# Kernel tuning notes

Measured on AMD Instinct MI355X. Metric: run time of the kernel, lower is better.

The kernel has to match this reference:

```python
import jax, jax.numpy as jnp
import numpy as np

TEMPERATURE = 8.0  # sqrt(d_k=64)
NEG_INF = -1.0e9   # matches masked_fill value in source


def setup_inputs() -> dict:
    key = jax.random.key(0)
    kq, kk, kv, km = jax.random.split(key, 4)
    B, H, T, C = 2, 16, 2048, 64
    q = jax.random.normal(kq, (B, H, T, C), dtype=jnp.float32)
    k = jax.random.normal(kk, (B, H, T, C), dtype=jnp.float32)
    v = jax.random.normal(kv, (B, H, T, C), dtype=jnp.float32)
    mask = jax.random.randint(km, (B, 1, T, T), 0, 2, dtype=jnp.int32)
    return {"q": q, "k": k, "v": v, "mask": mask}


def reference(q, k, v, mask):
    # attn = (q / temperature) @ k^T   -> [b, h, T, T]
    attn = jnp.einsum("bhqc,bhkc->bhqk", q / TEMPERATURE, k)
    attn = jnp.where(mask == 0, NEG_INF, attn)
    attn = jax.nn.softmax(attn, axis=-1)
    # dropout is identity in eval / deterministic reference
    output = jnp.einsum("bhqk,bhkc->bhqc", attn, v)
    return (output, attn)
```

## Files before the change

### kernel.cpp

```cpp
#include <hip/hip_runtime.h>
#include <stdint.h>
#include <stddef.h>

#define T_DIM 2048
#define C_DIM 64
#define SCALE_L2E 0.18033688011112042f

typedef __bf16 bf16x8 __attribute__((ext_vector_type(8)));
typedef float f32x4 __attribute__((ext_vector_type(4)));
typedef unsigned int u32x4 __attribute__((ext_vector_type(4)));
typedef unsigned int u32x2 __attribute__((ext_vector_type(2)));
typedef int i32x4 __attribute__((ext_vector_type(4)));
typedef unsigned short u16t;

#define PIDX(row, e) ((row) * T_DIM + ((e) ^ (((row) & 7) << 3)))

static __device__ __forceinline__ unsigned f2bf_bits(float f) {
  unsigned u = __builtin_bit_cast(unsigned, f);
  u += 0x7fffu + ((u >> 16) & 1u);
  return u >> 16;
}
static __device__ __forceinline__ bf16x8 asfrag(u32x4 u) {
  return __builtin_bit_cast(bf16x8, u);
}
static __device__ __forceinline__ bf16x8 pack8(f32x4 a, f32x4 b) {
  u32x4 u;
  u[0] = f2bf_bits(a[0]) | (f2bf_bits(a[1]) << 16);
  u[1] = f2bf_bits(a[2]) | (f2bf_bits(a[3]) << 16);
  u[2] = f2bf_bits(b[0]) | (f2bf_bits(b[1]) << 16);
  u[3] = f2bf_bits(b[2]) | (f2bf_bits(b[3]) << 16);
  return __builtin_bit_cast(bf16x8, u);
}
static __device__ __forceinline__ bf16x8 ld_cvt8(const float* p) {
  return pack8(*(const f32x4*)p, *(const f32x4*)(p + 4));
}

__global__ __launch_bounds__(256) void prep_kernel(const float* __restrict__ k,
                                                   const float* __restrict__ v,
                                                   u16t* __restrict__ kb,
                                                   u16t* __restrict__ vt) {
  if (blockIdx.x < 2048) {
    const size_t e0 = ((size_t)blockIdx.x * 256 + threadIdx.x) * 8;
    const float* src = k + e0;
    u32x4 u;
    f32x4 a = *(const f32x4*)src;
    f32x4 b = *(const f32x4*)(src + 4);
    u[0] = f2bf_bits(a[0]) | (f2bf_bits(a[1]) << 16);
    u[1] = f2bf_bits(a[2]) | (f2bf_bits(a[3]) << 16);
    u[2] = f2bf_bits(b[0]) | (f2bf_bits(b[1]) << 16);
    u[3] = f2bf_bits(b[2]) | (f2bf_bits(b[3]) << 16);
    *(u32x4*)(kb + e0) = u;
  } else {
    const int gid = (blockIdx.x - 2048) * 256 + threadIdx.x;
    const int bh = gid >> 11;
    const int j = gid & (T_DIM - 1);
    const float* src = v + ((size_t)bh * T_DIM + j) * C_DIM;
    u16t* dst = vt + (size_t)bh * (C_DIM * T_DIM) + j;
#pragma unroll
    for (int c0 = 0; c0 < C_DIM; c0 += 4) {
      f32x4 x = *(const f32x4*)(src + c0);
#pragma unroll
      for (int e = 0; e < 4; ++e)
        dst[(size_t)(c0 + e) * T_DIM] = (u16t)f2bf_bits(x[e]);
    }
  }
}

template <bool USE_PREP>
__global__ __launch_bounds__(256, 2) void attn_fwd(
    const float* __restrict__ qp, const float* __restrict__ kp,
    const float* __restrict__ vp, const int* __restrict__ maskp,
    const u16t* __restrict__ kbp, const u16t* __restrict__ vtp,
    float* __restrict__ outp, float* __restrict__ attnp) {
  __shared__ u16t Plds[16 * T_DIM];

  const int tid = threadIdx.x;
  const int wave = tid >> 6;
  const int lane = tid & 63;
  const int quad = lane >> 4;
  const int l15 = lane & 15;

  const int h = blockIdx.x & 15;
  const int qb = (blockIdx.x >> 4) & 127;
  const int b = blockIdx.x >> 11;
  const int bh = b * 16 + h;
  const int q0 = qb << 4;

  const float* qrow = qp + ((size_t)bh * T_DIM + q0 + l15) * C_DIM + quad * 8;
  const bf16x8 qf0 = ld_cvt8(qrow);
  const bf16x8 qf1 = ld_cvt8(qrow + 32);

  const u16t* kbbase = kbp + (size_t)bh * T_DIM * C_DIM;
  const float* kfbase = kp + (size_t)bh * T_DIM * C_DIM;
  const float* vfbase = vp + (size_t)bh * T_DIM * C_DIM;
  const u16t* vtrow = vtp + ((size_t)bh * C_DIM + l15) * T_DIM;
  const int* mrow = maskp + ((size_t)b * T_DIM + q0 + l15) * T_DIM;

  f32x4 ao0 = {0.f, 0.f, 0.f, 0.f};
  f32x4 ao1 = {0.f, 0.f, 0.f, 0.f};
  f32x4 ao2 = {0.f, 0.f, 0.f, 0.f};
  f32x4 ao3 = {0.f, 0.f, 0.f, 0.f};

#pragma unroll 1
  for (int s = 0; s < 16; ++s) {
    const int j0 = (s * 4 + wave) * 32;

    bf16x8 kA0, kA1, kB0, kB1;
    if (USE_PREP) {
      const u16t* ka = kbbase + (size_t)(j0 + l15) * C_DIM + quad * 8;
      kA0 = asfrag(*(const u32x4*)(ka));
      kA1 = asfrag(*(const u32x4*)(ka + 32));
      kB0 = asfrag(*(const u32x4*)(ka + 16 * C_DIM));
      kB1 = asfrag(*(const u32x4*)(ka + 16 * C_DIM + 32));
    } else {
      const float* ka = kfbase + (size_t)(j0 + l15) * C_DIM + quad * 8;
      kA0 = ld_cvt8(ka);
      kA1 = ld_cvt8(ka + 32);
      kB0 = ld_cvt8(ka + 16 * C_DIM);
      kB1 = ld_cvt8(ka + 16 * C_DIM + 32);
    }
    const i32x4 mA = *(const i32x4*)(mrow + j0 + quad * 4);
    const i32x4 mB = *(const i32x4*)(mrow + j0 + 16 + quad * 4);

    u32x4 vb0, vb1, vb2, vb3;
    if (USE_PREP) {
      const u16t* vt0 = vtrow + j0 + quad * 8;
      vb0 = *(const u32x4*)(vt0);
      vb1 = *(const u32x4*)(vt0 + 16 * T_DIM);
      vb2 = *(const u32x4*)(vt0 + 32 * T_DIM);
      vb3 = *(const u32x4*)(vt0 + 48 * T_DIM);
    } else {
      const float* g = vfbase + (size_t)(j0 + quad * 8) * C_DIM + l15;
      auto gather = [&](int c0) -> u32x4 {
        const float* p = g + c0;
        u32x4 r;
        r[0] = f2bf_bits(p[0]) | (f2bf_bits(p[C_DIM]) << 16);
        r[1] = f2bf_bits(p[2 * C_DIM]) | (f2bf_bits(p[3 * C_DIM]) << 16);
        r[2] = f2bf_bits(p[4 * C_DIM]) | (f2bf_bits(p[5 * C_DIM]) << 16);
        r[3] = f2bf_bits(p[6 * C_DIM]) | (f2bf_bits(p[7 * C_DIM]) << 16);
        return r;
      };
      vb0 = gather(0); vb1 = gather(16); vb2 = gather(32); vb3 = gather(48);
    }

    f32x4 sA = {0.f, 0.f, 0.f, 0.f};
    sA = __builtin_amdgcn_mfma_f32_16x16x32_bf16(kA0, qf0, sA, 0, 0, 0);
    sA = __builtin_amdgcn_mfma_f32_16x16x32_bf16(kA1, qf1, sA, 0, 0, 0);
    f32x4 sB = {0.f, 0.f, 0.f, 0.f};
    sB = __builtin_amdgcn_mfma_f32_16x16x32_bf16(kB0, qf0, sB, 0, 0, 0);
    sB = __builtin_amdgcn_mfma_f32_16x16x32_bf16(kB1, qf1, sB, 0, 0, 0);

    float a0 = mA[0] ? __builtin_exp2f(sA[0] * SCALE_L2E) : 0.f;
    float a1 = mA[1] ? __builtin_exp2f(sA[1] * SCALE_L2E) : 0.f;
    float a2 = mA[2] ? __builtin_exp2f(sA[2] * SCALE_L2E) : 0.f;
    float a3 = mA[3] ? __builtin_exp2f(sA[3] * SCALE_L2E) : 0.f;
    float b0 = mB[0] ? __builtin_exp2f(sB[0] * SCALE_L2E) : 0.f;
    float b1 = mB[1] ? __builtin_exp2f(sB[1] * SCALE_L2E) : 0.f;
    float b2 = mB[2] ? __builtin_exp2f(sB[2] * SCALE_L2E) : 0.f;
    float b3 = mB[3] ? __builtin_exp2f(sB[3] * SCALE_L2E) : 0.f;

    u32x2 wA, wB;
    wA[0] = f2bf_bits(a0) | (f2bf_bits(a1) << 16);
    wA[1] = f2bf_bits(a2) | (f2bf_bits(a3) << 16);
    wB[0] = f2bf_bits(b0) | (f2bf_bits(b1) << 16);
    wB[1] = f2bf_bits(b2) | (f2bf_bits(b3) << 16);
    *(u32x2*)&Plds[PIDX(l15, j0 + quad * 4)] = wA;
    *(u32x2*)&Plds[PIDX(l15, j0 + 16 + quad * 4)] = wB;

    const bf16x8 pa = asfrag(*(const u32x4*)&Plds[PIDX(l15, j0 + quad * 8)]);
    ao0 = __builtin_amdgcn_mfma_f32_16x16x32_bf16(pa, asfrag(vb0), ao0, 0, 0, 0);
    ao1 = __builtin_amdgcn_mfma_f32_16x16x32_bf16(pa, asfrag(vb1), ao1, 0, 0, 0);
    ao2 = __builtin_amdgcn_mfma_f32_16x16x32_bf16(pa, asfrag(vb2), ao2, 0, 0, 0);
    ao3 = __builtin_amdgcn_mfma_f32_16x16x32_bf16(pa, asfrag(vb3), ao3, 0, 0, 0);
  }

  __syncthreads();

  const int tq = tid >> 4;
  const int tj = (tid & 15) * 8;
  float ls = 0.f;
#pragma unroll
  for (int it = 0; it < 16; ++it) {
    const u32x4 pv = *(const u32x4*)&Plds[PIDX(tq, tj + it * 128)];
#pragma unroll
    for (int e = 0; e < 4; ++e) {
      ls += __builtin_bit_cast(float, pv[e] << 16);
      ls += __builtin_bit_cast(float, pv[e] & 0xffff0000u);
    }
  }
  ls += __shfl_xor(ls, 1, 64);
  ls += __shfl_xor(ls, 2, 64);
  ls += __shfl_xor(ls, 4, 64);
  ls += __shfl_xor(ls, 8, 64);
  const float rl = 1.0f / ls;

  float* arow = attnp + ((size_t)bh * T_DIM + q0 + tq) * T_DIM;
#pragma unroll
  for (int it = 0; it < 16; ++it) {
    const int j = tj + it * 128;
    const u32x4 pv = *(const u32x4*)&Plds[PIDX(tq, j)];
    f32x4 o0, o1;
#pragma unroll
    for (int e = 0; e < 2; ++e) {
      o0[2 * e] = __builtin_bit_cast(float, pv[e] << 16) * rl;
      o0[2 * e + 1] = __builtin_bit_cast(float, pv[e] & 0xffff0000u) * rl;
      o1[2 * e] = __builtin_bit_cast(float, pv[e + 2] << 16) * rl;
      o1[2 * e + 1] = __builtin_bit_cast(float, pv[e + 2] & 0xffff0000u) * rl;
    }
    *(f32x4*)(arow + j) = o0;
    *(f32x4*)(arow + j + 4) = o1;
  }
  __syncthreads();

  float* Of = (float*)Plds;
#pragma unroll
  for (int r = 0; r < 4; ++r) {
    const int qq = quad * 4 + r;
    float* dst = Of + wave * 1024 + qq * 64 + l15;
    dst[0] = ao0[r];
    dst[16] = ao1[r];
    dst[32] = ao2[r];
    dst[48] = ao3[r];
  }
  __syncthreads();
  {
    const int c = (tid & 15) * 4;
    f32x4 os = *(const f32x4*)&Of[tq * 64 + c];
    os += *(const f32x4*)&Of[1024 + tq * 64 + c];
    os += *(const f32x4*)&Of[2048 + tq * 64 + c];
    os += *(const f32x4*)&Of[3072 + tq * 64 + c];
    os *= rl;
    *(f32x4*)(outp + ((size_t)bh * T_DIM + q0 + tq) * C_DIM + c) = os;
  }
}

extern "C" void kernel_launch(void* const* d_in, const int* in_sizes, int n_in,
                              void* d_out, int out_size, void* d_ws, size_t ws_size,
                              hipStream_t stream) {
  const float* q = (const float*)d_in[0];
  const float* k = (const float*)d_in[1];
  const float* v = (const float*)d_in[2];
  const int* mask = (const int*)d_in[3];
  float* out = (float*)d_out;
  float* attn = out + (size_t)2 * 16 * T_DIM * C_DIM;

  const size_t n_elems = (size_t)2 * 16 * T_DIM * C_DIM;
  const size_t prep_bytes = 2 * n_elems * sizeof(u16t);
  if (ws_size >= prep_bytes) {
    u16t* kb = (u16t*)d_ws;
    u16t* vt = kb + n_elems;
    prep_kernel<<<2304, 256, 0, stream>>>(k, v, kb, vt);
    attn_fwd<true><<<4096, 256, 0, stream>>>(q, k, v, mask, kb, vt, out, attn);
  } else {
    attn_fwd<false><<<4096, 256, 0, stream>>>(q, k, v, mask, nullptr, nullptr, out, attn);
  }
}
```

Measured before the change: 881.9 us.

## Compute softmax row sums in a first pass and stream attn directly

Adds a first pass over all keys that computes QK^T and masked exp only to accumulate row sums, so the normalizer is known before the main pass. The main pass then writes normalized fp32 attention straight to global memory and stages only a small per-wave bf16 tile in LDS for the PV MFMA. This removes the 64KB full-row P buffer, shrinking LDS so more blocks fit per CU (launch bounds raised to 4). The cost is recomputing the QK^T MFMAs, re-reading the mask, and redoing the exps, plus attn stores that are less contiguous per lane.

```diff
diff --git a/kernel.cpp b/kernel.cpp
--- a/kernel.cpp
+++ b/kernel.cpp
@@ -5,6 +5,7 @@
 #define T_DIM 2048
 #define C_DIM 64
 #define SCALE_L2E 0.18033688011112042f
+#define STG_P 40
 
 typedef __bf16 bf16x8 __attribute__((ext_vector_type(8)));
 typedef float f32x4 __attribute__((ext_vector_type(4)));
@@ -12,8 +13,6 @@
 typedef unsigned int u32x2 __attribute__((ext_vector_type(2)));
 typedef int i32x4 __attribute__((ext_vector_type(4)));
 typedef unsigned short u16t;
-
-#define PIDX(row, e) ((row) * T_DIM + ((e) ^ (((row) & 7) << 3)))
 
 static __device__ __forceinline__ unsigned f2bf_bits(float f) {
   unsigned u = __builtin_bit_cast(unsigned, f);
@@ -67,12 +66,14 @@
 }
 
 template <bool USE_PREP>
-__global__ __launch_bounds__(256, 2) void attn_fwd(
+__global__ __launch_bounds__(256, 4) void attn_fwd(
     const float* __restrict__ qp, const float* __restrict__ kp,
     const float* __restrict__ vp, const int* __restrict__ maskp,
     const u16t* __restrict__ kbp, const u16t* __restrict__ vtp,
     float* __restrict__ outp, float* __restrict__ attnp) {
-  __shared__ u16t Plds[16 * T_DIM];
+  __shared__ float Of[4096];
+  __shared__ float rowsum[64];
+  __shared__ float rls[16];
 
   const int tid = threadIdx.x;
   const int wave = tid >> 6;
@@ -95,6 +96,58 @@
   const float* vfbase = vp + (size_t)bh * T_DIM * C_DIM;
   const u16t* vtrow = vtp + ((size_t)bh * C_DIM + l15) * T_DIM;
   const int* mrow = maskp + ((size_t)b * T_DIM + q0 + l15) * T_DIM;
+
+  float lsum = 0.f;
+#pragma unroll 1
+  for (int s = 0; s < 16; ++s) {
+    const int j0 = (s * 4 + wave) * 32;
+
+    bf16x8 kA0, kA1, kB0, kB1;
+    if (USE_PREP) {
+      const u16t* ka = kbbase + (size_t)(j0 + l15) * C_DIM + quad * 8;
+      kA0 = asfrag(*(const u32x4*)(ka));
+      kA1 = asfrag(*(const u32x4*)(ka + 32));
+      kB0 = asfrag(*(const u32x4*)(ka + 16 * C_DIM));
+      kB1 = asfrag(*(const u32x4*)(ka + 16 * C_DIM + 32));
+    } else {
+      const float* ka = kfbase + (size_t)(j0 + l15) * C_DIM + quad * 8;
+      kA0 = ld_cvt8(ka);
+      kA1 = ld_cvt8(ka + 32);
+      kB0 = ld_cvt8(ka + 16 * C_DIM);
+      kB1 = ld_cvt8(ka + 16 * C_DIM + 32);
+    }
+    const i32x4 mA = *(const i32x4*)(mrow + j0 + quad * 4);
+    const i32x4 mB = *(const i32x4*)(mrow + j0 + 16 + quad * 4);
+
+    f32x4 sA = {0.f, 0.f, 0.f, 0.f};
+    sA = __builtin_amdgcn_mfma_f32_16x16x32_bf16(kA0, qf0, sA, 0, 0, 0);
+    sA = __builtin_amdgcn_mfma_f32_16x16x32_bf16(kA1, qf1, sA, 0, 0, 0);
+    f32x4 sB = {0.f, 0.f, 0.f, 0.f};
+    sB = __builtin_amdgcn_mfma_f32_16x16x32_bf16(kB0, qf0, sB, 0, 0, 0);
+    sB = __builtin_amdgcn_mfma_f32_16x16x32_bf16(kB1, qf1, sB, 0, 0, 0);
+
+    lsum += mA[0] ? __builtin_exp2f(sA[0] * SCALE_L2E) : 0.f;
+    lsum += mA[1] ? __builtin_exp2f(sA[1] * SCALE_L2E) : 0.f;
+    lsum += mA[2] ? __builtin_exp2f(sA[2] * SCALE_L2E) : 0.f;
+    lsum += mA[3] ? __builtin_exp2f(sA[3] * SCALE_L2E) : 0.f;
+    lsum += mB[0] ? __builtin_exp2f(sB[0] * SCALE_L2E) : 0.f;
+    lsum += mB[1] ? __builtin_exp2f(sB[1] * SCALE_L2E) : 0.f;
+    lsum += mB[2] ? __builtin_exp2f(sB[2] * SCALE_L2E) : 0.f;
+    lsum += mB[3] ? __builtin_exp2f(sB[3] * SCALE_L2E) : 0.f;
+  }
+  lsum += __shfl_xor(lsum, 16, 64);
+  lsum += __shfl_xor(lsum, 32, 64);
+  if (quad == 0) rowsum[wave * 16 + l15] = lsum;
+  __syncthreads();
+  if (tid < 16)
+    rls[tid] = 1.0f / (rowsum[tid] + rowsum[16 + tid] + rowsum[32 + tid] +
+                       rowsum[48 + tid]);
+  __syncthreads();
+  const float rl_p = rls[l15];
+
+  u16t* const stg = (u16t*)Of + wave * (16 * STG_P);
+  float* const arow =
+      attnp + ((size_t)bh * T_DIM + q0 + l15) * T_DIM + quad * 4;
 
   f32x4 ao0 = {0.f, 0.f, 0.f, 0.f};
   f32x4 ao1 = {0.f, 0.f, 0.f, 0.f};
@@ -150,24 +203,30 @@
     sB = __builtin_amdgcn_mfma_f32_16x16x32_bf16(kB0, qf0, sB, 0, 0, 0);
     sB = __builtin_amdgcn_mfma_f32_16x16x32_bf16(kB1, qf1, sB, 0, 0, 0);
 
-    float a0 = mA[0] ? __builtin_exp2f(sA[0] * SCALE_L2E) : 0.f;
-    float a1 = mA[1] ? __builtin_exp2f(sA[1] * SCALE_L2E) : 0.f;
-    float a2 = mA[2] ? __builtin_exp2f(sA[2] * SCALE_L2E) : 0.f;
-    float a3 = mA[3] ? __builtin_exp2f(sA[3] * SCALE_L2E) : 0.f;
-    float b0 = mB[0] ? __builtin_exp2f(sB[0] * SCALE_L2E) : 0.f;
-    float b1 = mB[1] ? __builtin_exp2f(sB[1] * SCALE_L2E) : 0.f;
-    float b2 = mB[2] ? __builtin_exp2f(sB[2] * SCALE_L2E) : 0.f;
-    float b3 = mB[3] ? __builtin_exp2f(sB[3] * SCALE_L2E) : 0.f;
+    const float a0 = mA[0] ? __builtin_exp2f(sA[0] * SCALE_L2E) : 0.f;
+    const float a1 = mA[1] ? __builtin_exp2f(sA[1] * SCALE_L2E) : 0.f;
+    const float a2 = mA[2] ? __builtin_exp2f(sA[2] * SCALE_L2E) : 0.f;
+    const float a3 = mA[3] ? __builtin_exp2f(sA[3] * SCALE_L2E) : 0.f;
+    const float b0 = mB[0] ? __builtin_exp2f(sB[0] * SCALE_L2E) : 0.f;
+    const float b1 = mB[1] ? __builtin_exp2f(sB[1] * SCALE_L2E) : 0.f;
+    const float b2 = mB[2] ? __builtin_exp2f(sB[2] * SCALE_L2E) : 0.f;
+    const float b3 = mB[3] ? __builtin_exp2f(sB[3] * SCALE_L2E) : 0.f;
 
     u32x2 wA, wB;
     wA[0] = f2bf_bits(a0) | (f2bf_bits(a1) << 16);
     wA[1] = f2bf_bits(a2) | (f2bf_bits(a3) << 16);
     wB[0] = f2bf_bits(b0) | (f2bf_bits(b1) << 16);
     wB[1] = f2bf_bits(b2) | (f2bf_bits(b3) << 16);
-    *(u32x2*)&Plds[PIDX(l15, j0 + quad * 4)] = wA;
-    *(u32x2*)&Plds[PIDX(l15, j0 + 16 + quad * 4)] = wB;
-
-    const bf16x8 pa = asfrag(*(const u32x4*)&Plds[PIDX(l15, j0 + quad * 8)]);
+    *(u32x2*)&stg[l15 * STG_P + quad * 4] = wA;
+    *(u32x2*)&stg[l15 * STG_P + quad * 4 + 16] = wB;
+
+    f32x4 oA, oB;
+    oA[0] = a0 * rl_p; oA[1] = a1 * rl_p; oA[2] = a2 * rl_p; oA[3] = a3 * rl_p;
+    oB[0] = b0 * rl_p; oB[1] = b1 * rl_p; oB[2] = b2 * rl_p; oB[3] = b3 * rl_p;
+    *(f32x4*)(arow + j0) = oA;
+    *(f32x4*)(arow + j0 + 16) = oB;
+
+    const bf16x8 pa = asfrag(*(const u32x4*)&stg[l15 * STG_P + quad * 8]);
     ao0 = __builtin_amdgcn_mfma_f32_16x16x32_bf16(pa, asfrag(vb0), ao0, 0, 0, 0);
     ao1 = __builtin_amdgcn_mfma_f32_16x16x32_bf16(pa, asfrag(vb1), ao1, 0, 0, 0);
     ao2 = __builtin_amdgcn_mfma_f32_16x16x32_bf16(pa, asfrag(vb2), ao2, 0, 0, 0);
@@ -176,43 +235,6 @@
 
   __syncthreads();
 
-  const int tq = tid >> 4;
-  const int tj = (tid & 15) * 8;
-  float ls = 0.f;
-#pragma unroll
-  for (int it = 0; it < 16; ++it) {
-    const u32x4 pv = *(const u32x4*)&Plds[PIDX(tq, tj + it * 128)];
-#pragma unroll
-    for (int e = 0; e < 4; ++e) {
-      ls += __builtin_bit_cast(float, pv[e] << 16);
-      ls += __builtin_bit_cast(float, pv[e] & 0xffff0000u);
-    }
-  }
-  ls += __shfl_xor(ls, 1, 64);
-  ls += __shfl_xor(ls, 2, 64);
-  ls += __shfl_xor(ls, 4, 64);
-  ls += __shfl_xor(ls, 8, 64);
-  const float rl = 1.0f / ls;
-
-  float* arow = attnp + ((size_t)bh * T_DIM + q0 + tq) * T_DIM;
-#pragma unroll
-  for (int it = 0; it < 16; ++it) {
-    const int j = tj + it * 128;
-    const u32x4 pv = *(const u32x4*)&Plds[PIDX(tq, j)];
-    f32x4 o0, o1;
-#pragma unroll
-    for (int e = 0; e < 2; ++e) {
-      o0[2 * e] = __builtin_bit_cast(float, pv[e] << 16) * rl;
-      o0[2 * e + 1] = __builtin_bit_cast(float, pv[e] & 0xffff0000u) * rl;
-      o1[2 * e] = __builtin_bit_cast(float, pv[e + 2] << 16) * rl;
-      o1[2 * e + 1] = __builtin_bit_cast(float, pv[e + 2] & 0xffff0000u) * rl;
-    }
-    *(f32x4*)(arow + j) = o0;
-    *(f32x4*)(arow + j + 4) = o1;
-  }
-  __syncthreads();
-
-  float* Of = (float*)Plds;
 #pragma unroll
   for (int r = 0; r < 4; ++r) {
     const int qq = quad * 4 + r;
@@ -224,12 +246,13 @@
   }
   __syncthreads();
   {
+    const int tq = tid >> 4;
     const int c = (tid & 15) * 4;
     f32x4 os = *(const f32x4*)&Of[tq * 64 + c];
     os += *(const f32x4*)&Of[1024 + tq * 64 + c];
     os += *(const f32x4*)&Of[2048 + tq * 64 + c];
     os += *(const f32x4*)&Of[3072 + tq * 64 + c];
-    os *= rl;
+    os *= rls[tq];
     *(f32x4*)(outp + ((size_t)bh * T_DIM + q0 + tq) * C_DIM + c) = os;
   }
 }
```

Result: slower. 980.2 us (+11.2%).
